# Optimization experiments

Measured on AMD Instinct MI355X. Metric: run time of the kernel, lower is better.

## Reference

```python
import jax, jax.numpy as jnp
import numpy as np

IN_FEATURES = 2048
OUT_FEATURES = 8192
HARMONICS = 256
TWO_PI = 2.0 * np.pi


def setup_inputs() -> dict:
    key = jax.random.key(0)
    kx, kb, kp = jax.random.split(key, 3)
    x = jax.random.normal(kx, (4, 4096, IN_FEATURES), dtype=jnp.float32)
    # basis: randn then L2-normalized along in_features (dim=1), as in torch buffer init
    basis = jax.random.normal(kb, (HARMONICS, IN_FEATURES), dtype=jnp.float32)
    basis = basis / jnp.linalg.norm(basis, axis=1, keepdims=True)
    phase = jax.random.normal(kp, (OUT_FEATURES, HARMONICS), dtype=jnp.float32) * TWO_PI
    amp = jnp.ones((OUT_FEATURES, HARMONICS), dtype=jnp.float32) / HARMONICS
    return {"x": x, "basis": basis, "phase": phase, "amp": amp}


def reference(x, basis, phase, amp):
    # resonance = x @ basis.T : [..., harmonics]
    resonance = jnp.einsum("bsi,hi->bsh", x, basis)
    # Real part of (resonance + 0i) * (amp*cos(phase) + i*amp*sin(phase)) summed over h
    # collapses to resonance @ (amp * cos(phase)).T -- identical math, no complex dtype.
    w_real = amp * jnp.cos(phase)  # [out, harmonics]
    return jnp.einsum("bsh,oh->bso", resonance, w_real)
```

## Files before the change

### kernel.cpp

```cpp
#include <hip/hip_runtime.h>
#include <hip/hip_bf16.h>
#include <stdint.h>
#include <stddef.h>


typedef __bf16 bf16x8 __attribute__((ext_vector_type(8)));
typedef float  f32x4  __attribute__((ext_vector_type(4)));
typedef float  f32x16 __attribute__((ext_vector_type(16)));
typedef unsigned short u16x8 __attribute__((ext_vector_type(8)));

#define M_ROWS 16384
#define K_IN   2048
#define N_OUT  8192
#define N_HARM 256

__device__ inline unsigned short f2bf(float f) {
    union { float f; uint32_t u; } c; c.f = f;
    uint32_t u = c.u;
    uint32_t r = (u + 0x7fffu + ((u >> 16) & 1u)) >> 16;
    return (unsigned short)r;
}

__device__ inline bf16x8 cvt8(f32x4 a, f32x4 b) {
    bf16x8 r;
    r[0] = (__bf16)a[0]; r[1] = (__bf16)a[1]; r[2] = (__bf16)a[2]; r[3] = (__bf16)a[3];
    r[4] = (__bf16)b[0]; r[5] = (__bf16)b[1]; r[6] = (__bf16)b[2]; r[7] = (__bf16)b[3];
    return r;
}

#define GLDS(src, dst) \
    __builtin_amdgcn_global_load_lds((const __attribute__((address_space(1))) void*)(src), \
                                     (__attribute__((address_space(3))) void*)(dst), 16, 0, 0)

__global__ __launch_bounds__(256) void cvt_bf16(const float* __restrict__ in,
                                                unsigned short* __restrict__ out) {
    size_t i = ((size_t)blockIdx.x * 256 + threadIdx.x) * 8;
    f32x4 v0 = *(const f32x4*)(in + i);
    f32x4 v1 = *(const f32x4*)(in + i + 4);
    u16x8 o;
    o[0] = f2bf(v0[0]); o[1] = f2bf(v0[1]); o[2] = f2bf(v0[2]); o[3] = f2bf(v0[3]);
    o[4] = f2bf(v1[0]); o[5] = f2bf(v1[1]); o[6] = f2bf(v1[2]); o[7] = f2bf(v1[3]);
    *(u16x8*)(out + i) = o;
}

__global__ __launch_bounds__(256) void wreal_bf16(const float* __restrict__ phase,
                                                  const float* __restrict__ amp,
                                                  unsigned short* __restrict__ out) {
    size_t i = ((size_t)blockIdx.x * 256 + threadIdx.x) * 8;
    f32x4 p0 = *(const f32x4*)(phase + i);
    f32x4 p1 = *(const f32x4*)(phase + i + 4);
    f32x4 a0 = *(const f32x4*)(amp + i);
    f32x4 a1 = *(const f32x4*)(amp + i + 4);
    u16x8 o;
    o[0] = f2bf(a0[0] * cosf(p0[0])); o[1] = f2bf(a0[1] * cosf(p0[1]));
    o[2] = f2bf(a0[2] * cosf(p0[2])); o[3] = f2bf(a0[3] * cosf(p0[3]));
    o[4] = f2bf(a1[0] * cosf(p1[0])); o[5] = f2bf(a1[1] * cosf(p1[1]));
    o[6] = f2bf(a1[2] * cosf(p1[2])); o[7] = f2bf(a1[3] * cosf(p1[3]));
    *(u16x8*)(out + i) = o;
}

__global__ __launch_bounds__(256) void gemm1_fused(const float* __restrict__ A,
                                                   const unsigned short* __restrict__ B,
                                                   unsigned short* __restrict__ C) {
    __shared__ float          Asm[2][32 * 64];
    __shared__ unsigned short Bsm[2][256 * 64];

    const int tid  = threadIdx.x;
    const int lane = tid & 63;
    const int wv   = tid >> 6;
    const int bm0  = blockIdx.x * 32;

    const float* srcA[2];
#pragma unroll
    for (int q = 0; q < 2; ++q) {
        int L = q * 256 + tid;
        int r = L >> 4, p = L & 15;
        int c = p ^ (r & 15);
        srcA[q] = A + (size_t)(bm0 + r) * K_IN + c * 4;
    }
    const unsigned short* srcB[8];
#pragma unroll
    for (int q = 0; q < 8; ++q) {
        int L = q * 256 + tid;
        int r = L >> 3, p = L & 7;
        int c = p ^ (r & 7);
        srcB[q] = B + (size_t)r * K_IN + c * 8;
    }
    const int dA = wv * 256 + lane * 4;
    const int dB = wv * 512 + lane * 8;

    f32x16 acc[2];
#pragma unroll
    for (int nf = 0; nf < 2; ++nf)
#pragma unroll
        for (int e = 0; e < 16; ++e) acc[nf][e] = 0.f;

    const int r   = lane & 31;
    const int g   = lane >> 5;
    const int r15 = r & 15;
    const int colb = wv * 64;

#pragma unroll
    for (int q = 0; q < 2; ++q) GLDS(srcA[q], &Asm[0][q * 1024 + dA]);
#pragma unroll
    for (int q = 0; q < 8; ++q) GLDS(srcB[q], &Bsm[0][q * 2048 + dB]);
    __syncthreads();

    for (int t = 0; t < 32; ++t) {
        const int buf = t & 1;
        if (t + 1 < 32) {
            const int k0 = (t + 1) * 64;
#pragma unroll
            for (int q = 0; q < 2; ++q) GLDS(srcA[q] + k0, &Asm[buf ^ 1][q * 1024 + dA]);
#pragma unroll
            for (int q = 0; q < 8; ++q) GLDS(srcB[q] + k0, &Bsm[buf ^ 1][q * 2048 + dB]);
        }

        bf16x8 af[4];
#pragma unroll
        for (int ks = 0; ks < 4; ++ks) {
            const int c0 = g * 2 + ks * 4;
            f32x4 lo = *(const f32x4*)&Asm[buf][r * 64 + ((c0)     ^ r15) * 4];
            f32x4 hi = *(const f32x4*)&Asm[buf][r * 64 + ((c0 + 1) ^ r15) * 4];
            af[ks] = cvt8(lo, hi);
        }
#pragma unroll
        for (int nf = 0; nf < 2; ++nf) {
            const int rB = colb + nf * 32 + r;
            const int r7 = rB & 7;
#pragma unroll
            for (int ks = 0; ks < 4; ++ks) {
                const int cB = g + ks * 2;
                bf16x8 bfrag = *(const bf16x8*)&Bsm[buf][rB * 64 + (cB ^ r7) * 8];
                acc[nf] = __builtin_amdgcn_mfma_f32_32x32x16_bf16(af[ks], bfrag, acc[nf], 0, 0, 0);
            }
        }
        __syncthreads();
    }

#pragma unroll
    for (int nf = 0; nf < 2; ++nf)
#pragma unroll
        for (int reg = 0; reg < 16; ++reg) {
            int row = bm0 + (reg & 3) + 8 * (reg >> 2) + 4 * g;
            int col = colb + nf * 32 + r;
            C[(size_t)row * N_HARM + col] = f2bf(acc[nf][reg]);
        }
}

template<int K, int NCOLS>
__global__ __launch_bounds__(256) void gemm_bt(const unsigned short* __restrict__ A,
                                               const unsigned short* __restrict__ B,
                                               float* __restrict__ Cv) {
    __shared__ unsigned short As[2][128 * 32];
    __shared__ unsigned short Bs[2][128 * 32];

    const int tid  = threadIdx.x;
    const int lane = tid & 63;
    const int wv   = tid >> 6;
    const int wr   = wv >> 1;
    const int wc   = wv & 1;
    const int bm0  = blockIdx.y * 128;
    const int bn0  = blockIdx.x * 128;

    const int srow = tid >> 2;
    const int scol = (tid & 3) * 8;
    const unsigned short* gA0 = A + (size_t)(bm0 + srow) * K + scol;
    const unsigned short* gA1 = gA0 + (size_t)64 * K;
    const unsigned short* gB0 = B + (size_t)(bn0 + srow) * K + scol;
    const unsigned short* gB1 = gB0 + (size_t)64 * K;
    const int dL0 = wv * 512 + lane * 8;
    const int dL1 = 2048 + wv * 512 + lane * 8;

    f32x16 acc[2][2];
#pragma unroll
    for (int mi = 0; mi < 2; ++mi)
#pragma unroll
        for (int nj = 0; nj < 2; ++nj)
#pragma unroll
            for (int e = 0; e < 16; ++e) acc[mi][nj][e] = 0.f;

    const int r = lane & 31;
    const int g = lane >> 5;
    constexpr int NT = K / 32;

    GLDS(gA0, &As[0][dL0]); GLDS(gA1, &As[0][dL1]);
    GLDS(gB0, &Bs[0][dL0]); GLDS(gB1, &Bs[0][dL1]);
    __syncthreads();

    for (int t = 0; t < NT; ++t) {
        const int buf = t & 1;
        if (t + 1 < NT) {
            const int k0 = (t + 1) * 32;
            GLDS(gA0 + k0, &As[buf ^ 1][dL0]); GLDS(gA1 + k0, &As[buf ^ 1][dL1]);
            GLDS(gB0 + k0, &Bs[buf ^ 1][dL0]); GLDS(gB1 + k0, &Bs[buf ^ 1][dL1]);
        }

        bf16x8 af[2][2], bfr[2][2];
#pragma unroll
        for (int mi = 0; mi < 2; ++mi)
#pragma unroll
            for (int ks = 0; ks < 2; ++ks)
                af[mi][ks] = *(const bf16x8*)(&As[buf][(wr * 64 + mi * 32 + r) * 32 + ks * 16 + g * 8]);
#pragma unroll
        for (int nj = 0; nj < 2; ++nj)
#pragma unroll
            for (int ks = 0; ks < 2; ++ks)
                bfr[nj][ks] = *(const bf16x8*)(&Bs[buf][(wc * 64 + nj * 32 + r) * 32 + ks * 16 + g * 8]);

#pragma unroll
        for (int ks = 0; ks < 2; ++ks)
#pragma unroll
            for (int mi = 0; mi < 2; ++mi)
#pragma unroll
                for (int nj = 0; nj < 2; ++nj)
                    acc[mi][nj] = __builtin_amdgcn_mfma_f32_32x32x16_bf16(af[mi][ks], bfr[nj][ks], acc[mi][nj], 0, 0, 0);

        __syncthreads();
    }

#pragma unroll
    for (int mi = 0; mi < 2; ++mi)
#pragma unroll
        for (int nj = 0; nj < 2; ++nj)
#pragma unroll
            for (int reg = 0; reg < 16; ++reg) {
                int row = bm0 + wr * 64 + mi * 32 + (reg & 3) + 8 * (reg >> 2) + 4 * g;
                int col = bn0 + wc * 64 + nj * 32 + r;
                Cv[(size_t)row * NCOLS + col] = acc[mi][nj][reg];
            }
}

extern "C" void kernel_launch(void* const* d_in, const int* in_sizes, int n_in,
                              void* d_out, int out_size, void* d_ws, size_t ws_size,
                              hipStream_t stream) {
    const float* x     = (const float*)d_in[0];
    const float* basis = (const float*)d_in[1];
    const float* phase = (const float*)d_in[2];
    const float* amp   = (const float*)d_in[3];
    float* out = (float*)d_out;

    char* ws = (char*)d_ws;
    unsigned short* bb  = (unsigned short*)(ws);
    unsigned short* wrb = (unsigned short*)(ws + 1048576);
    unsigned short* rb  = (unsigned short*)(ws + 5242880);

    cvt_bf16<<<dim3(256), dim3(256), 0, stream>>>(basis, bb);
    wreal_bf16<<<dim3(1024), dim3(256), 0, stream>>>(phase, amp, wrb);

    gemm1_fused<<<dim3(M_ROWS / 32), dim3(256), 0, stream>>>(x, bb, rb);
    gemm_bt<256, 8192><<<dim3(N_OUT / 128, M_ROWS / 128), dim3(256), 0, stream>>>(rb, wrb, out);
}
```

Measured before the change: 211.9 us.

## Repack GEMM2 operands into MFMA fragment layout and load directly to registers

Writes the W_real matrix and the resonance intermediate in a pre-swizzled fragment-major layout, adding a repack kernel for the resonance. The second GEMM then loads MFMA fragments straight from global memory into registers with a three-deep prefetch, with no LDS staging or barriers. Blocks are remapped with a swizzle for L2 locality. The cost is an extra kernel launch plus a copy of the 8 MB intermediate, and heavier reliance on cache hits for operands that are reused across blocks.

```diff
diff --git a/kernel.cpp b/kernel.cpp
--- a/kernel.cpp
+++ b/kernel.cpp
@@ -43,10 +43,11 @@
     *(u16x8*)(out + i) = o;
 }
 
-__global__ __launch_bounds__(256) void wreal_bf16(const float* __restrict__ phase,
-                                                  const float* __restrict__ amp,
-                                                  unsigned short* __restrict__ out) {
-    size_t i = ((size_t)blockIdx.x * 256 + threadIdx.x) * 8;
+__global__ __launch_bounds__(256) void wreal_swz(const float* __restrict__ phase,
+                                                 const float* __restrict__ amp,
+                                                 unsigned short* __restrict__ out) {
+    int gid = blockIdx.x * 256 + threadIdx.x;
+    size_t i = (size_t)gid * 8;
     f32x4 p0 = *(const f32x4*)(phase + i);
     f32x4 p1 = *(const f32x4*)(phase + i + 4);
     f32x4 a0 = *(const f32x4*)(amp + i);
@@ -56,7 +57,26 @@
     o[2] = f2bf(a0[2] * cosf(p0[2])); o[3] = f2bf(a0[3] * cosf(p0[3]));
     o[4] = f2bf(a1[0] * cosf(p1[0])); o[5] = f2bf(a1[1] * cosf(p1[1]));
     o[6] = f2bf(a1[2] * cosf(p1[2])); o[7] = f2bf(a1[3] * cosf(p1[3]));
-    *(u16x8*)(out + i) = o;
+    int orow = gid >> 5;
+    int j    = gid & 31;
+    int kt   = j >> 1;
+    int kh   = j & 1;
+    int ch   = (orow & 31) + 32 * kh;
+    size_t dst = (((size_t)(orow >> 5) * 16 + kt) * 64 + ch) * 8;
+    *(u16x8*)(out + dst) = o;
+}
+
+__global__ __launch_bounds__(256) void repack_rb(const unsigned short* __restrict__ rb,
+                                                 unsigned short* __restrict__ out) {
+    int gid = blockIdx.x * 256 + threadIdx.x;
+    int m = gid >> 5;
+    int j = gid & 31;
+    u16x8 v = *(const u16x8*)(rb + (size_t)m * N_HARM + j * 8);
+    int kt = j >> 1;
+    int kh = j & 1;
+    int ch = (m & 31) + 32 * kh;
+    size_t dst = (((size_t)(m >> 5) * 16 + kt) * 64 + ch) * 8;
+    *(u16x8*)(out + dst) = v;
 }
 
 __global__ __launch_bounds__(256) void gemm1_fused(const float* __restrict__ A,
@@ -148,29 +168,28 @@
         }
 }
 
-template<int K, int NCOLS>
-__global__ __launch_bounds__(256) void gemm_bt(const unsigned short* __restrict__ A,
-                                               const unsigned short* __restrict__ B,
-                                               float* __restrict__ Cv) {
-    __shared__ unsigned short As[2][128 * 32];
-    __shared__ unsigned short Bs[2][128 * 32];
-
+__global__ __launch_bounds__(256) void gemm2_reg(const unsigned short* __restrict__ Aswz,
+                                                 const unsigned short* __restrict__ Bswz,
+                                                 float* __restrict__ Cv) {
     const int tid  = threadIdx.x;
     const int lane = tid & 63;
     const int wv   = tid >> 6;
-    const int wr   = wv >> 1;
-    const int wc   = wv & 1;
-    const int bm0  = blockIdx.y * 128;
-    const int bn0  = blockIdx.x * 128;
-
-    const int srow = tid >> 2;
-    const int scol = (tid & 3) * 8;
-    const unsigned short* gA0 = A + (size_t)(bm0 + srow) * K + scol;
-    const unsigned short* gA1 = gA0 + (size_t)64 * K;
-    const unsigned short* gB0 = B + (size_t)(bn0 + srow) * K + scol;
-    const unsigned short* gB1 = gB0 + (size_t)64 * K;
-    const int dL0 = wv * 512 + lane * 8;
-    const int dL1 = 2048 + wv * 512 + lane * 8;
+
+    const int flat = blockIdx.x;
+    const int swz  = (flat & 7) * 1024 + (flat >> 3);
+    const int bm0  = (swz >> 6) * 128 + (wv >> 1) * 64;
+    const int bn0  = (swz & 63) * 128 + (wv & 1) * 64;
+
+    const int mt0 = bm0 >> 5;
+    const int nt0 = bn0 >> 5;
+
+    const unsigned short* Ab[2];
+    const unsigned short* Bb[2];
+#pragma unroll
+    for (int i = 0; i < 2; ++i) {
+        Ab[i] = Aswz + ((size_t)(mt0 + i) * 16) * 512 + lane * 8;
+        Bb[i] = Bswz + ((size_t)(nt0 + i) * 16) * 512 + lane * 8;
+    }
 
     f32x16 acc[2][2];
 #pragma unroll
@@ -179,55 +198,44 @@
         for (int nj = 0; nj < 2; ++nj)
 #pragma unroll
             for (int e = 0; e < 16; ++e) acc[mi][nj][e] = 0.f;
+
+    bf16x8 fa[3][2], fb[3][2];
+#pragma unroll
+    for (int s = 0; s < 2; ++s)
+#pragma unroll
+        for (int i = 0; i < 2; ++i) {
+            fa[s][i] = *(const bf16x8*)(Ab[i] + s * 512);
+            fb[s][i] = *(const bf16x8*)(Bb[i] + s * 512);
+        }
+
+#pragma unroll
+    for (int ki = 0; ki < 16; ++ki) {
+        const int cur = ki % 3;
+        if (ki + 2 < 16) {
+            const int nx = (ki + 2) % 3;
+#pragma unroll
+            for (int i = 0; i < 2; ++i) {
+                fa[nx][i] = *(const bf16x8*)(Ab[i] + (ki + 2) * 512);
+                fb[nx][i] = *(const bf16x8*)(Bb[i] + (ki + 2) * 512);
+            }
+        }
+        acc[0][0] = __builtin_amdgcn_mfma_f32_32x32x16_bf16(fa[cur][0], fb[cur][0], acc[0][0], 0, 0, 0);
+        acc[0][1] = __builtin_amdgcn_mfma_f32_32x32x16_bf16(fa[cur][0], fb[cur][1], acc[0][1], 0, 0, 0);
+        acc[1][0] = __builtin_amdgcn_mfma_f32_32x32x16_bf16(fa[cur][1], fb[cur][0], acc[1][0], 0, 0, 0);
+        acc[1][1] = __builtin_amdgcn_mfma_f32_32x32x16_bf16(fa[cur][1], fb[cur][1], acc[1][1], 0, 0, 0);
+    }
 
     const int r = lane & 31;
     const int g = lane >> 5;
-    constexpr int NT = K / 32;
-
-    GLDS(gA0, &As[0][dL0]); GLDS(gA1, &As[0][dL1]);
-    GLDS(gB0, &Bs[0][dL0]); GLDS(gB1, &Bs[0][dL1]);
-    __syncthreads();
-
-    for (int t = 0; t < NT; ++t) {
-        const int buf = t & 1;
-        if (t + 1 < NT) {
-            const int k0 = (t + 1) * 32;
-            GLDS(gA0 + k0, &As[buf ^ 1][dL0]); GLDS(gA1 + k0, &As[buf ^ 1][dL1]);
-            GLDS(gB0 + k0, &Bs[buf ^ 1][dL0]); GLDS(gB1 + k0, &Bs[buf ^ 1][dL1]);
-        }
-
-        bf16x8 af[2][2], bfr[2][2];
-#pragma unroll
-        for (int mi = 0; mi < 2; ++mi)
-#pragma unroll
-            for (int ks = 0; ks < 2; ++ks)
-                af[mi][ks] = *(const bf16x8*)(&As[buf][(wr * 64 + mi * 32 + r) * 32 + ks * 16 + g * 8]);
+#pragma unroll
+    for (int mi = 0; mi < 2; ++mi)
 #pragma unroll
         for (int nj = 0; nj < 2; ++nj)
 #pragma unroll
-            for (int ks = 0; ks < 2; ++ks)
-                bfr[nj][ks] = *(const bf16x8*)(&Bs[buf][(wc * 64 + nj * 32 + r) * 32 + ks * 16 + g * 8]);
-
-#pragma unroll
-        for (int ks = 0; ks < 2; ++ks)
-#pragma unroll
-            for (int mi = 0; mi < 2; ++mi)
-#pragma unroll
-                for (int nj = 0; nj < 2; ++nj)
-                    acc[mi][nj] = __builtin_amdgcn_mfma_f32_32x32x16_bf16(af[mi][ks], bfr[nj][ks], acc[mi][nj], 0, 0, 0);
-
-        __syncthreads();
-    }
-
-#pragma unroll
-    for (int mi = 0; mi < 2; ++mi)
-#pragma unroll
-        for (int nj = 0; nj < 2; ++nj)
-#pragma unroll
             for (int reg = 0; reg < 16; ++reg) {
-                int row = bm0 + wr * 64 + mi * 32 + (reg & 3) + 8 * (reg >> 2) + 4 * g;
-                int col = bn0 + wc * 64 + nj * 32 + r;
-                Cv[(size_t)row * NCOLS + col] = acc[mi][nj][reg];
+                int row = bm0 + mi * 32 + (reg & 3) + 8 * (reg >> 2) + 4 * g;
+                int col = bn0 + nj * 32 + r;
+                Cv[(size_t)row * N_OUT + col] = acc[mi][nj][reg];
             }
 }
 
@@ -241,13 +249,15 @@
     float* out = (float*)d_out;
 
     char* ws = (char*)d_ws;
-    unsigned short* bb  = (unsigned short*)(ws);
-    unsigned short* wrb = (unsigned short*)(ws + 1048576);
-    unsigned short* rb  = (unsigned short*)(ws + 5242880);
+    unsigned short* bb    = (unsigned short*)(ws);
+    unsigned short* bswz  = (unsigned short*)(ws + 1048576);
+    unsigned short* rb    = (unsigned short*)(ws + 5242880);
+    unsigned short* aswz  = (unsigned short*)(ws + 13631488);
 
     cvt_bf16<<<dim3(256), dim3(256), 0, stream>>>(basis, bb);
-    wreal_bf16<<<dim3(1024), dim3(256), 0, stream>>>(phase, amp, wrb);
+    wreal_swz<<<dim3(1024), dim3(256), 0, stream>>>(phase, amp, bswz);
 
     gemm1_fused<<<dim3(M_ROWS / 32), dim3(256), 0, stream>>>(x, bb, rb);
-    gemm_bt<256, 8192><<<dim3(N_OUT / 128, M_ROWS / 128), dim3(256), 0, stream>>>(rb, wrb, out);
-}
+    repack_rb<<<dim3(2048), dim3(256), 0, stream>>>(rb, aswz);
+    gemm2_reg<<<dim3(8192), dim3(256), 0, stream>>>(aswz, bswz, out);
+}
```

After: 270.2 us. 1.27x slower.

## Triple-buffer second GEMM with XOR-swizzled LDS layout and explicit vmcnt waits

Applied to the files above, without the earlier changes.

Replaces the double-buffered second GEMM with a three-stage LDS pipeline. Loads run two tiles ahead and are gated by explicit s_waitcnt vmcnt plus a raw s_barrier instead of __syncthreads, and the K=256 loop is fully unrolled. The shared-memory tile layout is changed to an XOR-swizzled arrangement to cut LDS bank conflicts on fragment reads. It uses more LDS per block, which may lower occupancy, and it relies on hand-counted outstanding loads being correct.

```diff
diff --git a/kernel.cpp b/kernel.cpp
--- a/kernel.cpp
+++ b/kernel.cpp
@@ -148,12 +148,11 @@
         }
 }
 
-template<int K, int NCOLS>
-__global__ __launch_bounds__(256) void gemm_bt(const unsigned short* __restrict__ A,
-                                               const unsigned short* __restrict__ B,
-                                               float* __restrict__ Cv) {
-    __shared__ unsigned short As[2][128 * 32];
-    __shared__ unsigned short Bs[2][128 * 32];
+__global__ __launch_bounds__(256) void gemm2_pipe(const unsigned short* __restrict__ A,
+                                                  const unsigned short* __restrict__ B,
+                                                  float* __restrict__ Cv) {
+    __shared__ unsigned short As[3][4096];
+    __shared__ unsigned short Bs[3][4096];
 
     const int tid  = threadIdx.x;
     const int lane = tid & 63;
@@ -163,14 +162,25 @@
     const int bm0  = blockIdx.y * 128;
     const int bn0  = blockIdx.x * 128;
 
-    const int srow = tid >> 2;
-    const int scol = (tid & 3) * 8;
-    const unsigned short* gA0 = A + (size_t)(bm0 + srow) * K + scol;
-    const unsigned short* gA1 = gA0 + (size_t)64 * K;
-    const unsigned short* gB0 = B + (size_t)(bn0 + srow) * K + scol;
-    const unsigned short* gB1 = gB0 + (size_t)64 * K;
-    const int dL0 = wv * 512 + lane * 8;
-    const int dL1 = 2048 + wv * 512 + lane * 8;
+    const unsigned short* srcA[2];
+    const unsigned short* srcB[2];
+#pragma unroll
+    for (int q = 0; q < 2; ++q) {
+        int L = q * 256 + tid;
+        int lrow = L >> 3, chp = L & 7;
+        int ch = chp ^ (lrow & 7);
+        int m = (ch >> 2) * 64 + lrow;
+        int k = (ch & 3) * 8;
+        srcA[q] = A + (size_t)(bm0 + m) * N_HARM + k;
+        srcB[q] = B + (size_t)(bn0 + m) * N_HARM + k;
+    }
+    const int dst = tid * 8;
+
+#define STAGE2(b, t) do { \
+    GLDS(srcA[0] + (t) * 32, &As[b][dst]);        \
+    GLDS(srcA[1] + (t) * 32, &As[b][2048 + dst]); \
+    GLDS(srcB[0] + (t) * 32, &Bs[b][dst]);        \
+    GLDS(srcB[1] + (t) * 32, &Bs[b][2048 + dst]); } while (0)
 
     f32x16 acc[2][2];
 #pragma unroll
@@ -180,44 +190,38 @@
 #pragma unroll
             for (int e = 0; e < 16; ++e) acc[mi][nj][e] = 0.f;
 
-    const int r = lane & 31;
-    const int g = lane >> 5;
-    constexpr int NT = K / 32;
-
-    GLDS(gA0, &As[0][dL0]); GLDS(gA1, &As[0][dL1]);
-    GLDS(gB0, &Bs[0][dL0]); GLDS(gB1, &Bs[0][dL1]);
-    __syncthreads();
-
-    for (int t = 0; t < NT; ++t) {
-        const int buf = t & 1;
-        if (t + 1 < NT) {
-            const int k0 = (t + 1) * 32;
-            GLDS(gA0 + k0, &As[buf ^ 1][dL0]); GLDS(gA1 + k0, &As[buf ^ 1][dL1]);
-            GLDS(gB0 + k0, &Bs[buf ^ 1][dL0]); GLDS(gB1 + k0, &Bs[buf ^ 1][dL1]);
-        }
-
-        bf16x8 af[2][2], bfr[2][2];
+    const int r  = lane & 31;
+    const int g  = lane >> 5;
+    const int r7 = r & 7;
+
+    STAGE2(0, 0);
+    STAGE2(1, 1);
+
+#pragma unroll
+    for (int t = 0; t < 8; ++t) {
+        if (t == 7) { asm volatile("s_waitcnt vmcnt(0)" ::: "memory"); }
+        else        { asm volatile("s_waitcnt vmcnt(4)" ::: "memory"); }
+        __builtin_amdgcn_s_barrier();
+        if (t + 2 < 8) STAGE2((t + 2) % 3, t + 2);
+
+        const int b = t % 3;
+        bf16x8 af[2][2], bfx[2][2];
 #pragma unroll
         for (int mi = 0; mi < 2; ++mi)
 #pragma unroll
-            for (int ks = 0; ks < 2; ++ks)
-                af[mi][ks] = *(const bf16x8*)(&As[buf][(wr * 64 + mi * 32 + r) * 32 + ks * 16 + g * 8]);
-#pragma unroll
-        for (int nj = 0; nj < 2; ++nj)
-#pragma unroll
-            for (int ks = 0; ks < 2; ++ks)
-                bfr[nj][ks] = *(const bf16x8*)(&Bs[buf][(wc * 64 + nj * 32 + r) * 32 + ks * 16 + g * 8]);
-
+            for (int ks = 0; ks < 2; ++ks) {
+                af[mi][ks]  = *(const bf16x8*)&As[b][(mi * 32 + r) * 64 + ((wr * 4 + ks * 2 + g) ^ r7) * 8];
+                bfx[mi][ks] = *(const bf16x8*)&Bs[b][(mi * 32 + r) * 64 + ((wc * 4 + ks * 2 + g) ^ r7) * 8];
+            }
 #pragma unroll
         for (int ks = 0; ks < 2; ++ks)
 #pragma unroll
             for (int mi = 0; mi < 2; ++mi)
 #pragma unroll
                 for (int nj = 0; nj < 2; ++nj)
-                    acc[mi][nj] = __builtin_amdgcn_mfma_f32_32x32x16_bf16(af[mi][ks], bfr[nj][ks], acc[mi][nj], 0, 0, 0);
-
-        __syncthreads();
-    }
+                    acc[mi][nj] = __builtin_amdgcn_mfma_f32_32x32x16_bf16(af[mi][ks], bfx[nj][ks], acc[mi][nj], 0, 0, 0);
+    }
+#undef STAGE2
 
 #pragma unroll
     for (int mi = 0; mi < 2; ++mi)
@@ -227,7 +231,7 @@
             for (int reg = 0; reg < 16; ++reg) {
                 int row = bm0 + wr * 64 + mi * 32 + (reg & 3) + 8 * (reg >> 2) + 4 * g;
                 int col = bn0 + wc * 64 + nj * 32 + r;
-                Cv[(size_t)row * NCOLS + col] = acc[mi][nj][reg];
+                Cv[(size_t)row * N_OUT + col] = acc[mi][nj][reg];
             }
 }
 
@@ -249,5 +253,5 @@
     wreal_bf16<<<dim3(1024), dim3(256), 0, stream>>>(phase, amp, wrb);
 
     gemm1_fused<<<dim3(M_ROWS / 32), dim3(256), 0, stream>>>(x, bb, rb);
-    gemm_bt<256, 8192><<<dim3(N_OUT / 128, M_ROWS / 128), dim3(256), 0, stream>>>(rb, wrb, out);
-}
+    gemm2_pipe<<<dim3(N_OUT / 128, M_ROWS / 128), dim3(256), 0, stream>>>(rb, wrb, out);
+}
```

Result: no change. 209.8 us (-1.0%).
